# Performance work log

Hardware: AMD Instinct MI355X
Metric: run time of the kernel (lower is better)

## Reference

```python
import jax, jax.numpy as jnp
import numpy as np

N = 100000   # nodes
E = 1600000  # edges
IN = 128
H = 64
OUT = 10
NG = 128     # number of graphs
EPS = 1e-5


def _lin(k, o, i):
    kw, kb = jax.random.split(k)
    bound = 1.0 / np.sqrt(i)
    W = jax.random.uniform(kw, (o, i), jnp.float32, -bound, bound)
    b = jax.random.uniform(kb, (o,), jnp.float32, -bound, bound)
    return W, b


def setup_inputs() -> dict:
    key = jax.random.key(0)
    ks = jax.random.split(key, 10)
    x = jax.random.normal(ks[0], (N, IN), jnp.float32)
    edge_index = jax.random.randint(ks[1], (2, E), 0, N, dtype=jnp.int64)
    batch = jnp.sort(jax.random.randint(ks[2], (N,), 0, NG, dtype=jnp.int64))
    W1, b1 = _lin(ks[3], H, IN)
    W2, b2 = _lin(ks[4], H, H)
    W3, b3 = _lin(ks[5], H, H)
    Wc1, bc1 = _lin(ks[6], H, H)
    Wc2, bc2 = _lin(ks[7], OUT, H)
    ones = jnp.ones((H,), jnp.float32)
    zeros = jnp.zeros((H,), jnp.float32)
    return {
        "x": x, "edge_index": edge_index, "batch": batch,
        "W1": W1, "b1": b1, "g1": ones, "be1": zeros,
        "W2": W2, "b2": b2, "g2": ones, "be2": zeros,
        "W3": W3, "b3": b3, "g3": ones, "be3": zeros,
        "Wc1": Wc1, "bc1": bc1, "Wc2": Wc2, "bc2": bc2,
    }


def reference(x, edge_index, batch,
              W1, b1, g1, be1, W2, b2, g2, be2, W3, b3, g3, be3,
              Wc1, bc1, Wc2, bc2):
    n = x.shape[0]
    src, dst = edge_index[0], edge_index[1]
    loop = jnp.arange(n, dtype=src.dtype)
    src_a = jnp.concatenate([src, loop])  # [E+N] with self loops
    dst_a = jnp.concatenate([dst, loop])
    # degree via scatter-add (self loops included -> deg >= 1)
    deg = jax.ops.segment_sum(jnp.ones_like(dst_a, jnp.float32), dst_a, num_segments=n)
    norm = (deg[src_a] * deg[dst_a]) ** -0.5
    norm = jnp.where(jnp.isinf(norm), 0.0, norm)  # guard deg==0 (faithful to source)

    def conv(h, W, b):
        h = h @ W.T + b                       # [N, H]
        msg = h[src_a] * norm[:, None]        # gather + scale  [E+N, H]
        return jax.ops.segment_sum(msg, dst_a, num_segments=n)  # scatter-add

    def bn_relu(h, g, be):
        mu = h.mean(0)
        var = h.var(0)  # biased variance (torch BN training mode)
        return jax.nn.relu(g * (h - mu) / jnp.sqrt(var + EPS) + be)

    for (W, b, g, be) in [(W1, b1, g1, be1), (W2, b2, g2, be2), (W3, b3, g3, be3)]:
        x = bn_relu(conv(x, W, b), g, be)

    pool = jax.ops.segment_sum(x, batch, num_segments=NG)  # readout='sum'
    h = jax.nn.relu(pool @ Wc1.T + bc1)
    return h @ Wc2.T + bc2
```

## Files before the change

### kernel.cpp

```cpp
#include <hip/hip_runtime.h>
#include <hip/hip_bf16.h>


#define NN 100000
#define NE 1600000
#define INF_ 128
#define HF 64
#define OUTF 10
#define NG 128
#define NBUCK 391
#define NBLKP 512
#define CPB (NE / NBLKP)
#define NPART 32
#define PARTF (3 * NPART * 128 + NG * HF)

typedef short bf16x8 __attribute__((ext_vector_type(8)));
typedef float f32x4 __attribute__((ext_vector_type(4)));

static __device__ __forceinline__ unsigned short f2bf(float x) {
    unsigned int b = __float_as_uint(x);
    b += 0x7FFFu + ((b >> 16) & 1u);
    return (unsigned short)(b >> 16);
}
static __device__ __forceinline__ float bf2f(unsigned short u) {
    return __uint_as_float(((unsigned int)u) << 16);
}
static __device__ __forceinline__ float bflo(unsigned int u) {
    return __uint_as_float(u << 16);
}
static __device__ __forceinline__ float bfhi(unsigned int u) {
    return __uint_as_float(u & 0xffff0000u);
}

__global__ __launch_bounds__(256) void k_front(const int* __restrict__ dst,
                                               int* __restrict__ gcount,
                                               const float* __restrict__ W1f,
                                               const float* __restrict__ W2f,
                                               const float* __restrict__ W3f,
                                               unsigned short* __restrict__ wp0,
                                               unsigned short* __restrict__ wp1,
                                               unsigned short* __restrict__ wp2,
                                               float* __restrict__ part) {
    int t = threadIdx.x, b = blockIdx.x;
    if (b < NBLKP) {
        __shared__ int cnt[NBUCK];
        for (int i = t; i < NBUCK; i += 256) cnt[i] = 0;
        __syncthreads();
        int beg = b * CPB, end = beg + CPB;
        for (int i = beg + t; i < end; i += 256) atomicAdd(&cnt[dst[i] >> 8], 1);
        __syncthreads();
        for (int i = t; i < NBUCK; i += 256) gcount[i * NBLKP + b] = cnt[i];
    } else if (b < NBLKP + 8) {
        int bb = b - NBLKP;
        const float* W;
        unsigned short* P;
        int K, base;
        if (bb < 4)      { W = W1f; P = wp0; K = INF_; base = bb; }
        else if (bb < 6) { W = W2f; P = wp1; K = HF;   base = bb - 4; }
        else             { W = W3f; P = wp2; K = HF;   base = bb - 6; }
        int q = base * 256 + t;
        int nchunk = (K >> 5) << 8;
        if (q >= nchunk) return;
        int kb = q >> 8;
        int gq = (q >> 6) & 3;
        int ch = q & 63;
        const float* wr = W + (size_t)ch * K;
        unsigned int u[4];
#pragma unroll
        for (int i = 0; i < 4; ++i) {
            int e0 = 2 * i, e1 = 2 * i + 1;
            int k0 = kb * 32 + 4 * gq + (e0 & 3) + 16 * (e0 >> 2);
            int k1 = kb * 32 + 4 * gq + (e1 & 3) + 16 * (e1 >> 2);
            u[i] = (unsigned int)f2bf(wr[k0]) | ((unsigned int)f2bf(wr[k1]) << 16);
        }
        *(uint4*)(P + (size_t)q * 8) = make_uint4(u[0], u[1], u[2], u[3]);
    } else {
        int i = (b - NBLKP - 8) * 256 + t;
        if (i < PARTF) part[i] = 0.f;
    }
}

__global__ void k_scan1(const int* __restrict__ cnt, int* __restrict__ ro,
                        int* __restrict__ bsum, int n) {
    __shared__ int ts[256];
    int base = blockIdx.x * 1024 + threadIdx.x * 4;
    int v[4], s = 0;
#pragma unroll
    for (int k = 0; k < 4; ++k) {
        int idx = base + k;
        v[k] = (idx < n) ? cnt[idx] : 0;
        s += v[k];
    }
    ts[threadIdx.x] = s;
    __syncthreads();
    for (int off = 1; off < 256; off <<= 1) {
        int t = (threadIdx.x >= off) ? ts[threadIdx.x - off] : 0;
        __syncthreads();
        ts[threadIdx.x] += t;
        __syncthreads();
    }
    int ex = ts[threadIdx.x] - s;
    if (threadIdx.x == 255) bsum[blockIdx.x] = ts[255];
#pragma unroll
    for (int k = 0; k < 4; ++k) {
        int idx = base + k;
        if (idx < n) ro[idx] = ex;
        ex += v[k];
    }
}

__global__ void k_scan2(int* __restrict__ bsum, int nb) {
    __shared__ int ts[256];
    int i = threadIdx.x;
    int v = (i < nb) ? bsum[i] : 0;
    ts[i] = v;
    __syncthreads();
    for (int off = 1; off < 256; off <<= 1) {
        int t = (i >= off) ? ts[i - off] : 0;
        __syncthreads();
        ts[i] += t;
        __syncthreads();
    }
    if (i < nb) bsum[i] = ts[i] - v;
}

__global__ __launch_bounds__(256) void kB_part(const int* __restrict__ src,
                                               const int* __restrict__ dst,
                                               const int* __restrict__ goff,
                                               const int* __restrict__ bsum,
                                               int* __restrict__ tmp) {
    __shared__ int cur[NBUCK];
    int t = threadIdx.x, blk = blockIdx.x;
    for (int i = t; i < NBUCK; i += 256) {
        int idx = i * NBLKP + blk;
        cur[i] = goff[idx] + bsum[idx >> 10];
    }
    __syncthreads();
    int beg = blk * CPB, end = beg + CPB;
    for (int i = beg + t; i < end; i += 256) {
        int d = dst[i];
        int pos = atomicAdd(&cur[d >> 8], 1);
        tmp[pos] = ((d & 255) << 17) | src[i];
    }
}

__global__ __launch_bounds__(256) void kC_build(const int* __restrict__ goff,
                                                const int* __restrict__ bsum,
                                                int* __restrict__ tmp,
                                                int* __restrict__ ss,
                                                int* __restrict__ ro,
                                                float* __restrict__ rdeg, int E) {
    __shared__ int cnt[256];
    __shared__ int ts[256];
    __shared__ int cur[256];
    int t = threadIdx.x, b = blockIdx.x;
    int i0 = b * NBLKP;
    int beg = goff[i0] + bsum[i0 >> 10];
    int end = E;
    if (b + 1 < NBUCK) {
        int i1 = (b + 1) * NBLKP;
        end = goff[i1] + bsum[i1 >> 10];
    }
    cnt[t] = 0;
    __syncthreads();
    for (int i = beg + t; i < end; i += 256) atomicAdd(&cnt[tmp[i] >> 17], 1);
    __syncthreads();
    int s = cnt[t];
    ts[t] = s;
    __syncthreads();
    for (int off = 1; off < 256; off <<= 1) {
        int v = (t >= off) ? ts[t - off] : 0;
        __syncthreads();
        ts[t] += v;
        __syncthreads();
    }
    int p = beg + ts[t] - s;
    cur[t] = p;
    int node = (b << 8) + t;
    if (node < NN) {
        ro[node] = p;
        rdeg[node] = rsqrtf((float)s + 1.f);
    } else if (node == NN) {
        ro[NN] = p;
    }
    __syncthreads();
    for (int i = beg + t; i < end; i += 256) {
        int pk = tmp[i];
        int pos = atomicAdd(&cur[pk >> 17], 1);
        ss[pos] = pk & 0x1FFFF;
    }
}

template<int K, bool BN>
__global__ __launch_bounds__(256) void k_gemm_mfma(const float* __restrict__ Xf,
                                                   const unsigned short* __restrict__ Xh,
                                                   const unsigned short* __restrict__ Wp,
                                                   const float* __restrict__ bias,
                                                   const float* __restrict__ rdeg,
                                                   const float* __restrict__ SP,
                                                   const float* __restrict__ g,
                                                   const float* __restrict__ be,
                                                   unsigned short* __restrict__ Hs, int n) {
    constexpr int KB = K / 32;
    constexpr int RB = K * 2;
    __shared__ __align__(16) char raw[64 * 68 * 4];
    __shared__ float sa_l[64], sb_l[64];
    const int t = threadIdx.x;
    const int w = t >> 6;
    const int c = t & 15;
    const int gq = (t >> 4) & 3;
    const int r0 = blockIdx.x * 64;

    if (BN && t < 64) {
        float s = 0.f, q = 0.f;
#pragma unroll
        for (int p = 0; p < NPART; ++p) {
            s += SP[p * 128 + t];
            q += SP[p * 128 + 64 + t];
        }
        float n_ = (float)NN;
        float mu = s / n_;
        float var = q / n_ - mu * mu;
        float a = g[t] * rsqrtf(var + 1e-5f);
        sa_l[t] = a;
        sb_l[t] = be[t] - mu * a;
    }
    __syncthreads();

    {
        int r = t >> 2, q = t & 3;
        int row = r0 + r;
        int x_swz = (r & 7) << 4;
        if (BN) {
            int ch0 = q * 16;
            uint4 u0 = make_uint4(0, 0, 0, 0), u1 = make_uint4(0, 0, 0, 0);
            if (row < n) {
                const uint4* p = (const uint4*)(Xh + (size_t)row * 64 + ch0);
                u0 = p[0];
                u1 = p[1];
            }
            unsigned int uin[8] = {u0.x, u0.y, u0.z, u0.w, u1.x, u1.y, u1.z, u1.w};
            unsigned int uo[8];
#pragma unroll
            for (int j = 0; j < 8; ++j) {
                int chl = ch0 + 2 * j, chh = chl + 1;
                float v0 = fmaxf(fmaf(sa_l[chl], bflo(uin[j]), sb_l[chl]), 0.f);
                float v1 = fmaxf(fmaf(sa_l[chh], bfhi(uin[j]), sb_l[chh]), 0.f);
                uo[j] = (unsigned int)f2bf(v0) | ((unsigned int)f2bf(v1) << 16);
            }
            int b0 = r * RB + q * 32;
            *(uint4*)(raw + ((b0) ^ x_swz)) = make_uint4(uo[0], uo[1], uo[2], uo[3]);
            *(uint4*)(raw + ((b0 + 16) ^ x_swz)) = make_uint4(uo[4], uo[5], uo[6], uo[7]);
        } else {
            int ch0 = q * 32;
#pragma unroll
            for (int j2 = 0; j2 < 4; ++j2) {
                float4 a = make_float4(0.f, 0.f, 0.f, 0.f), b = make_float4(0.f, 0.f, 0.f, 0.f);
                if (row < n) {
                    const float4* p = (const float4*)(Xf + (size_t)row * K + ch0 + j2 * 8);
                    a = p[0];
                    b = p[1];
                }
                unsigned int q0 = (unsigned int)f2bf(a.x) | ((unsigned int)f2bf(a.y) << 16);
                unsigned int q1 = (unsigned int)f2bf(a.z) | ((unsigned int)f2bf(a.w) << 16);
                unsigned int q2 = (unsigned int)f2bf(b.x) | ((unsigned int)f2bf(b.y) << 16);
                unsigned int q3 = (unsigned int)f2bf(b.z) | ((unsigned int)f2bf(b.w) << 16);
                int b0 = r * RB + ch0 * 2 + j2 * 16;
                *(uint4*)(raw + (b0 ^ x_swz)) = make_uint4(q0, q1, q2, q3);
            }
        }
    }
    __syncthreads();

    bf16x8 af[KB];
    {
        int r = 16 * w + c;
        int rb = r * RB;
        int swz = (r & 7) << 4;
#pragma unroll
        for (int kb = 0; kb < KB; ++kb) {
            int off = rb + kb * 64 + gq * 8;
            uint2 u0 = *(const uint2*)(raw + (off ^ swz));
            uint2 u1 = *(const uint2*)(raw + ((off + 32) ^ swz));
            union { uint4 u; bf16x8 v; } cv;
            cv.u = make_uint4(u0.x, u0.y, u1.x, u1.y);
            af[kb] = cv.v;
        }
    }
    const uint4* wq = (const uint4*)Wp;
    f32x4 acc[4];
#pragma unroll
    for (int nn_ = 0; nn_ < 4; ++nn_) {
        acc[nn_] = (f32x4){0.f, 0.f, 0.f, 0.f};
#pragma unroll
        for (int kb = 0; kb < KB; ++kb) {
            union { uint4 u; bf16x8 v; } cw;
            cw.u = wq[(kb * 4 + gq) * 64 + nn_ * 16 + c];
            acc[nn_] = __builtin_amdgcn_mfma_f32_16x16x32_bf16(af[kb], cw.v, acc[nn_], 0, 0, 0);
        }
    }

    __syncthreads();
    float* outb = (float*)raw;
    float rv[4];
#pragma unroll
    for (int i = 0; i < 4; ++i) {
        int rg = r0 + 16 * w + 4 * gq + i;
        rv[i] = (rg < n) ? rdeg[rg] : 0.f;
    }
#pragma unroll
    for (int nn_ = 0; nn_ < 4; ++nn_) {
        int col = 16 * nn_ + c;
        float bz = bias[col];
#pragma unroll
        for (int i = 0; i < 4; ++i)
            outb[(16 * w + 4 * gq + i) * 68 + col] = (acc[nn_][i] + bz) * rv[i];
    }
    __syncthreads();
    {
        int r = t >> 2, q = t & 3;
        int row = r0 + r;
        if (row < n) {
            const float* src = outb + r * 68 + q * 16;
            unsigned int u[8];
#pragma unroll
            for (int j = 0; j < 8; ++j)
                u[j] = (unsigned int)f2bf(src[2 * j]) | ((unsigned int)f2bf(src[2 * j + 1]) << 16);
            uint4* p = (uint4*)(Hs + (size_t)row * HF + q * 16);
            p[0] = make_uint4(u[0], u[1], u[2], u[3]);
            p[1] = make_uint4(u[4], u[5], u[6], u[7]);
        }
    }
}

__global__ __launch_bounds__(256) void k_agg(const int* __restrict__ ro,
                                             const int* __restrict__ ss,
                                             const unsigned short* __restrict__ Hs,
                                             const float* __restrict__ rdeg,
                                             unsigned short* __restrict__ V16,
                                             float* __restrict__ partial, int n) {
    __shared__ float red[4][128];
    int t = threadIdx.x;
    int wid = blockIdx.x * 4 + (t >> 6);
    int lane = t & 63;
    int sub = lane >> 4;
    int lq = lane & 15;
    int c4 = lq * 4;
    int node = wid * 4 + sub;
    bool vn = node < n;
    int safe = vn ? node : 0;
    int beg = 0, d = 0;
    if (vn) {
        beg = ro[node];
        d = ro[node + 1] - beg;
    }
    float4 acc = make_float4(0.f, 0.f, 0.f, 0.f);
    if (vn) {
        uint2 u = *(const uint2*)(Hs + ((size_t)node << 6) + c4);
        acc.x = bflo(u.x); acc.y = bfhi(u.x); acc.z = bflo(u.y); acc.w = bfhi(u.y);
    }
    int dm = d;
    dm = max(dm, __shfl_xor(dm, 16));
    dm = max(dm, __shfl_xor(dm, 32));
    for (int it = 0; it < dm; it += 16) {
        int myidx = (it + lq < d) ? ss[beg + it + lq] : -1;
        int sidx[16];
        float msk[16];
#pragma unroll
        for (int k = 0; k < 16; ++k) {
            int s = __shfl(myidx, (sub << 4) + k);
            sidx[k] = (s >= 0) ? s : safe;
            msk[k] = (s >= 0) ? 1.f : 0.f;
        }
        uint2 u[16];
#pragma unroll
        for (int k = 0; k < 16; ++k)
            u[k] = *(const uint2*)(Hs + ((size_t)sidx[k] << 6) + c4);
#pragma unroll
        for (int k = 0; k < 16; ++k) {
            acc.x = fmaf(msk[k], bflo(u[k].x), acc.x);
            acc.y = fmaf(msk[k], bfhi(u[k].x), acc.y);
            acc.z = fmaf(msk[k], bflo(u[k].y), acc.z);
            acc.w = fmaf(msk[k], bfhi(u[k].y), acc.w);
        }
    }
    float rv = vn ? rdeg[node] : 0.f;
    float v0 = acc.x * rv, v1 = acc.y * rv, v2 = acc.z * rv, v3 = acc.w * rv;
    if (vn) {
        unsigned int p0 = (unsigned int)f2bf(v0) | ((unsigned int)f2bf(v1) << 16);
        unsigned int p1 = (unsigned int)f2bf(v2) | ((unsigned int)f2bf(v3) << 16);
        *(uint2*)(V16 + ((size_t)node << 6) + c4) = make_uint2(p0, p1);
    }
    float s0 = v0, s1 = v1, s2 = v2, s3 = v3;
    float q0 = v0 * v0, q1 = v1 * v1, q2 = v2 * v2, q3 = v3 * v3;
#pragma unroll
    for (int m = 16; m <= 32; m <<= 1) {
        s0 += __shfl_xor(s0, m); s1 += __shfl_xor(s1, m);
        s2 += __shfl_xor(s2, m); s3 += __shfl_xor(s3, m);
        q0 += __shfl_xor(q0, m); q1 += __shfl_xor(q1, m);
        q2 += __shfl_xor(q2, m); q3 += __shfl_xor(q3, m);
    }
    if (sub == 0) {
        int w = t >> 6;
        red[w][c4 + 0] = s0; red[w][c4 + 1] = s1;
        red[w][c4 + 2] = s2; red[w][c4 + 3] = s3;
        red[w][64 + c4 + 0] = q0; red[w][64 + c4 + 1] = q1;
        red[w][64 + c4 + 2] = q2; red[w][64 + c4 + 3] = q3;
    }
    __syncthreads();
    if (t < 128) {
        float r = red[0][t] + red[1][t] + red[2][t] + red[3][t];
        atomicAdd(&partial[(blockIdx.x & (NPART - 1)) * 128 + t], r);
    }
}

__global__ __launch_bounds__(256) void k_pool2(const unsigned short* __restrict__ V16,
                                               const float* __restrict__ SP,
                                               const float* __restrict__ g,
                                               const float* __restrict__ be,
                                               const int* __restrict__ batch,
                                               float* __restrict__ pool, int n) {
    __shared__ float sa_l[64], sb_l[64];
    int t = threadIdx.x;
    if (t < 64) {
        float s = 0.f, q = 0.f;
#pragma unroll
        for (int p = 0; p < NPART; ++p) {
            s += SP[p * 128 + t];
            q += SP[p * 128 + 64 + t];
        }
        float n_ = (float)NN;
        float mu = s / n_;
        float var = q / n_ - mu * mu;
        float a = g[t] * rsqrtf(var + 1e-5f);
        sa_l[t] = a;
        sb_l[t] = be[t] - mu * a;
    }
    __syncthreads();
    int wid = blockIdx.x * 4 + (t >> 6);
    int r0 = wid * 64;
    if (r0 >= n) return;
    int lane = t & 63;
    float sa = sa_l[lane], sb = sb_l[lane];
    int rend = min(r0 + 64, n);
    int cur = batch[r0];
    float s = 0.f;
    for (int r = r0; r < rend; ++r) {
        int b = batch[r];
        if (b != cur) {
            atomicAdd(&pool[(size_t)cur * HF + lane], s);
            s = 0.f;
            cur = b;
        }
        float v = bf2f(V16[(size_t)r * HF + lane]);
        s += fmaxf(fmaf(sa, v, sb), 0.f);
    }
    atomicAdd(&pool[(size_t)cur * HF + lane], s);
}

__global__ void k_cls(const float* __restrict__ pool, const float* __restrict__ Wc1,
                      const float* __restrict__ bc1, const float* __restrict__ Wc2,
                      const float* __restrict__ bc2, float* __restrict__ out) {
    __shared__ float pl[HF], hr[HF];
    int g = blockIdx.x, c = threadIdx.x;
    pl[c] = pool[g * HF + c];
    __syncthreads();
    float h = bc1[c];
#pragma unroll
    for (int k = 0; k < HF; ++k) h = fmaf(pl[k], Wc1[c * HF + k], h);
    hr[c] = fmaxf(h, 0.f);
    __syncthreads();
    if (c < OUTF) {
        float o = bc2[c];
#pragma unroll
        for (int k = 0; k < HF; ++k) o = fmaf(hr[k], Wc2[c * HF + k], o);
        out[g * OUTF + c] = o;
    }
}

extern "C" void kernel_launch(void* const* d_in, const int* in_sizes, int n_in,
                              void* d_out, int out_size, void* d_ws, size_t ws_size,
                              hipStream_t stream) {
    const float* x = (const float*)d_in[0];
    const int* edge = (const int*)d_in[1];
    const int* batch = (const int*)d_in[2];
    const float* W1 = (const float*)d_in[3];
    const float* b1 = (const float*)d_in[4];
    const float* g1 = (const float*)d_in[5];
    const float* be1 = (const float*)d_in[6];
    const float* W2 = (const float*)d_in[7];
    const float* b2 = (const float*)d_in[8];
    const float* g2 = (const float*)d_in[9];
    const float* be2 = (const float*)d_in[10];
    const float* W3 = (const float*)d_in[11];
    const float* b3 = (const float*)d_in[12];
    const float* g3 = (const float*)d_in[13];
    const float* be3 = (const float*)d_in[14];
    const float* Wc1 = (const float*)d_in[15];
    const float* bc1 = (const float*)d_in[16];
    const float* Wc2 = (const float*)d_in[17];
    const float* bc2 = (const float*)d_in[18];
    float* out = (float*)d_out;

    const int* src = edge;
    const int* dst = edge + NE;

    const size_t N64 = (size_t)NN * HF;
    const int NGC = NBUCK * NBLKP;
    unsigned short* V16 = (unsigned short*)d_ws;
    unsigned short* Hs = V16 + N64;
    float* rdeg = (float*)(Hs + N64);
    float* part = rdeg + NN;
    float* pool = part + 3 * NPART * 128;
    int* gcount = (int*)(pool + (size_t)NG * HF);
    int* goff = gcount + NGC;
    int* bsum = goff + NGC;
    int* ro = bsum + 256;
    int* tmp = ro + NN + 1;
    int* ss = tmp + NE;
    unsigned short* wp0 = (unsigned short*)(ss + NE);
    unsigned short* wp1 = wp0 + 8192;
    unsigned short* wp2 = wp1 + 4096;

    k_front<<<NBLKP + 8 + (PARTF + 255) / 256, 256, 0, stream>>>(
        dst, gcount, W1, W2, W3, wp0, wp1, wp2, part);

    const int nblk = (NGC + 1023) / 1024;
    k_scan1<<<nblk, 256, 0, stream>>>(gcount, goff, bsum, NGC);
    k_scan2<<<1, 256, 0, stream>>>(bsum, nblk);
    kB_part<<<NBLKP, 256, 0, stream>>>(src, dst, goff, bsum, tmp);
    kC_build<<<NBUCK, 256, 0, stream>>>(goff, bsum, tmp, ss, ro, rdeg, NE);

    const unsigned short* gWp[3] = {wp0, wp1, wp2};
    const float* gb[3] = {b1, b2, b3};
    const float* gg[3] = {g1, g2, g3};
    const float* gbe[3] = {be1, be2, be3};

    const int tileblk = (NN + 63) / 64;
    const int aggblk = (NN + 15) / 16;
    const int poolblk = ((NN + 63) / 64 + 3) / 4;

    for (int l = 0; l < 3; ++l) {
        if (l == 0)
            k_gemm_mfma<INF_, false><<<tileblk, 256, 0, stream>>>(x, (const unsigned short*)0,
                                                                  gWp[0], gb[0], rdeg, part,
                                                                  gg[0], gbe[0], Hs, NN);
        else
            k_gemm_mfma<HF, true><<<tileblk, 256, 0, stream>>>((const float*)0, V16,
                                                               gWp[l], gb[l], rdeg,
                                                               part + (l - 1) * NPART * 128,
                                                               gg[l - 1], gbe[l - 1], Hs, NN);
        k_agg<<<aggblk, 256, 0, stream>>>(ro, ss, Hs, rdeg, V16,
                                          part + l * NPART * 128, NN);
        if (l == 2)
            k_pool2<<<poolblk, 256, 0, stream>>>(V16, part + 2 * NPART * 128,
                                                 gg[2], gbe[2], batch, pool, NN);
    }

    k_cls<<<NG, HF, 0, stream>>>(pool, Wc1, bc1, Wc2, bc2, out);
}
```

Measured before the change: 226.6 us.

## Split aggregation feature columns across two blocks with 8 lanes per node

The aggregation kernel now assigns each node's 64 features to two separate blocks, one per 32-column half. Each block uses 8 lanes per node and covers 32 nodes, and neighbor indices are processed in chunks of 8 instead of 16. The goal is more concurrent nodes per wave and less idle work when neighbor counts are uneven, which should help latency hiding on the gather. In exchange, the edge index list and degree values are read twice, and there are more blocks and more partial-sum atomics.

```diff
diff --git a/kernel.cpp b/kernel.cpp
--- a/kernel.cpp
+++ b/kernel.cpp
@@ -339,14 +339,16 @@
                                              const float* __restrict__ rdeg,
                                              unsigned short* __restrict__ V16,
                                              float* __restrict__ partial, int n) {
-    __shared__ float red[4][128];
+    __shared__ float red[4][64];
     int t = threadIdx.x;
-    int wid = blockIdx.x * 4 + (t >> 6);
+    int h = blockIdx.x & 1;
+    int blk = blockIdx.x >> 1;
+    int wv = t >> 6;
     int lane = t & 63;
-    int sub = lane >> 4;
-    int lq = lane & 15;
-    int c4 = lq * 4;
-    int node = wid * 4 + sub;
+    int sub = lane >> 3;
+    int lq = lane & 7;
+    int co = h * 32 + lq * 4;
+    int node = blk * 32 + wv * 8 + sub;
     bool vn = node < n;
     int safe = vn ? node : 0;
     int beg = 0, d = 0;
@@ -356,28 +358,29 @@
     }
     float4 acc = make_float4(0.f, 0.f, 0.f, 0.f);
     if (vn) {
-        uint2 u = *(const uint2*)(Hs + ((size_t)node << 6) + c4);
+        uint2 u = *(const uint2*)(Hs + ((size_t)node << 6) + co);
         acc.x = bflo(u.x); acc.y = bfhi(u.x); acc.z = bflo(u.y); acc.w = bfhi(u.y);
     }
     int dm = d;
+    dm = max(dm, __shfl_xor(dm, 8));
     dm = max(dm, __shfl_xor(dm, 16));
     dm = max(dm, __shfl_xor(dm, 32));
-    for (int it = 0; it < dm; it += 16) {
+    for (int it = 0; it < dm; it += 8) {
         int myidx = (it + lq < d) ? ss[beg + it + lq] : -1;
-        int sidx[16];
-        float msk[16];
-#pragma unroll
-        for (int k = 0; k < 16; ++k) {
-            int s = __shfl(myidx, (sub << 4) + k);
+        int sidx[8];
+        float msk[8];
+#pragma unroll
+        for (int k = 0; k < 8; ++k) {
+            int s = __shfl(myidx, (sub << 3) + k);
             sidx[k] = (s >= 0) ? s : safe;
             msk[k] = (s >= 0) ? 1.f : 0.f;
         }
-        uint2 u[16];
-#pragma unroll
-        for (int k = 0; k < 16; ++k)
-            u[k] = *(const uint2*)(Hs + ((size_t)sidx[k] << 6) + c4);
-#pragma unroll
-        for (int k = 0; k < 16; ++k) {
+        uint2 u[8];
+#pragma unroll
+        for (int k = 0; k < 8; ++k)
+            u[k] = *(const uint2*)(Hs + ((size_t)sidx[k] << 6) + co);
+#pragma unroll
+        for (int k = 0; k < 8; ++k) {
             acc.x = fmaf(msk[k], bflo(u[k].x), acc.x);
             acc.y = fmaf(msk[k], bfhi(u[k].x), acc.y);
             acc.z = fmaf(msk[k], bflo(u[k].y), acc.z);
@@ -389,28 +392,31 @@
     if (vn) {
         unsigned int p0 = (unsigned int)f2bf(v0) | ((unsigned int)f2bf(v1) << 16);
         unsigned int p1 = (unsigned int)f2bf(v2) | ((unsigned int)f2bf(v3) << 16);
-        *(uint2*)(V16 + ((size_t)node << 6) + c4) = make_uint2(p0, p1);
+        *(uint2*)(V16 + ((size_t)node << 6) + co) = make_uint2(p0, p1);
     }
     float s0 = v0, s1 = v1, s2 = v2, s3 = v3;
     float q0 = v0 * v0, q1 = v1 * v1, q2 = v2 * v2, q3 = v3 * v3;
 #pragma unroll
-    for (int m = 16; m <= 32; m <<= 1) {
+    for (int m = 8; m <= 32; m <<= 1) {
         s0 += __shfl_xor(s0, m); s1 += __shfl_xor(s1, m);
         s2 += __shfl_xor(s2, m); s3 += __shfl_xor(s3, m);
         q0 += __shfl_xor(q0, m); q1 += __shfl_xor(q1, m);
         q2 += __shfl_xor(q2, m); q3 += __shfl_xor(q3, m);
     }
     if (sub == 0) {
-        int w = t >> 6;
-        red[w][c4 + 0] = s0; red[w][c4 + 1] = s1;
-        red[w][c4 + 2] = s2; red[w][c4 + 3] = s3;
-        red[w][64 + c4 + 0] = q0; red[w][64 + c4 + 1] = q1;
-        red[w][64 + c4 + 2] = q2; red[w][64 + c4 + 3] = q3;
-    }
-    __syncthreads();
-    if (t < 128) {
+        red[wv][lq * 4 + 0] = s0; red[wv][lq * 4 + 1] = s1;
+        red[wv][lq * 4 + 2] = s2; red[wv][lq * 4 + 3] = s3;
+        red[wv][32 + lq * 4 + 0] = q0; red[wv][32 + lq * 4 + 1] = q1;
+        red[wv][32 + lq * 4 + 2] = q2; red[wv][32 + lq * 4 + 3] = q3;
+    }
+    __syncthreads();
+    if (t < 64) {
         float r = red[0][t] + red[1][t] + red[2][t] + red[3][t];
-        atomicAdd(&partial[(blockIdx.x & (NPART - 1)) * 128 + t], r);
+        int slot = blockIdx.x & (NPART - 1);
+        int dest;
+        if (t < 32) dest = slot * 128 + h * 32 + t;
+        else        dest = slot * 128 + 64 + h * 32 + (t - 32);
+        atomicAdd(&partial[dest], r);
     }
 }
 
@@ -537,7 +543,7 @@
     const float* gbe[3] = {be1, be2, be3};
 
     const int tileblk = (NN + 63) / 64;
-    const int aggblk = (NN + 15) / 16;
+    const int aggblk = 2 * ((NN + 31) / 32);
     const int poolblk = ((NN + 63) / 64 + 3) / 4;
 
     for (int l = 0; l < 3; ++l) {
```

After: 290.6 us. 1.28x slower.
